# Performance work log

Measured on AMD Instinct MI355X. Metric: run time of the kernel, lower is better.

Reference implementation:

```python
import jax, jax.numpy as jnp
import numpy as np

N_NODES = 100000
N_EDGES = 1600000
IN_FEATS = 128
H_FEATS = 64
PROP_STEP = 2


def _gcn_propagate(x, src, dst, num_nodes, add_self_loops):
    """PyG gcn_norm + scatter-add propagation. edge_weight=None -> all ones.
    GCNConv uses add_self_loops=True; LGConv uses add_self_loops=False."""
    if add_self_loops:
        loop = jnp.arange(num_nodes, dtype=src.dtype)
        src = jnp.concatenate([src, loop])
        dst = jnp.concatenate([dst, loop])
    # degree over destination nodes (flow source_to_target)
    deg = jax.ops.segment_sum(jnp.ones(src.shape, dtype=x.dtype), dst,
                              num_segments=num_nodes)
    dinv = jnp.where(deg > 0, jax.lax.rsqrt(deg), jnp.zeros_like(deg))
    norm = dinv[src] * dinv[dst]                      # [E]
    msg = x[src] * norm[:, None]                      # [E, F] gather + scale
    return jax.ops.segment_sum(msg, dst, num_segments=num_nodes)  # [N, F]


def setup_inputs() -> dict:
    key = jax.random.key(0)
    k1, k2, k3 = jax.random.split(key, 3)
    edge_index = jax.random.randint(k1, (2, N_EDGES), 0, N_NODES, dtype=jnp.int32)
    in_feat = jax.random.normal(k2, (N_NODES, IN_FEATS), dtype=jnp.float32)
    # GCNConv linear weight (bias=False), stored as [in, out]
    W1 = jax.random.normal(k3, (IN_FEATS, H_FEATS), dtype=jnp.float32) * (1.0 / np.sqrt(IN_FEATS))
    alphas = jnp.ones((PROP_STEP,), dtype=jnp.float32)  # nn.Parameter(ones(prop_step))
    return {"edge_index": edge_index, "in_feat": in_feat, "W1": W1, "alphas": alphas}


def reference(edge_index, in_feat, W1, alphas):
    src, dst = edge_index[0], edge_index[1]
    num_nodes = in_feat.shape[0]
    alpha = jax.nn.softmax(alphas)
    # conv1 = GCNConv(bias=False): linear transform then normalized propagation with self loops
    h = _gcn_propagate(in_feat @ W1, src, dst, num_nodes, add_self_loops=True)
    res = h * alpha[0]
    # remaining steps: LGConv (no self loops), norm/relu disabled by default
    for i in range(1, PROP_STEP):
        h = _gcn_propagate(h, src, dst, num_nodes, add_self_loops=False)
        res = res + h * alpha[i]
    return res
```

## Files before the change

kernel.cpp:

```cpp
#include <hip/hip_runtime.h>

#define N_NODES 100000
#define N_EDGES 1600000
#define IN_F 128
#define H_F 64
#define ZROW N_NODES

#define BSH 10
#define BNODES 1024
#define NBKT 98
#define EPB 4096
#define BCAP 20000
#define SCAP 28192

typedef short short8 __attribute__((ext_vector_type(8)));
typedef float floatx4 __attribute__((ext_vector_type(4)));

union U16x8 { short8 v; unsigned short us[8]; unsigned int u[4]; };

static __device__ __forceinline__ unsigned short f2bf(float f) {
    unsigned int u = __float_as_uint(f);
    unsigned int r = (u + 0x7FFFu + ((u >> 16) & 1u)) >> 16;
    return (unsigned short)r;
}
static __device__ __forceinline__ float bflo(unsigned int u) {
    return __uint_as_float(u << 16);
}
static __device__ __forceinline__ float bfhi(unsigned int u) {
    return __uint_as_float(u & 0xFFFF0000u);
}
static __device__ __forceinline__ unsigned int pk2(float a, float b) {
    return (unsigned int)f2bf(a) | ((unsigned int)f2bf(b) << 16);
}

__global__ __launch_bounds__(256) void initwpack_kernel(const float* __restrict__ W,
                                                        unsigned int* __restrict__ wfrag,
                                                        int* __restrict__ ccur,
                                                        unsigned int* __restrict__ XsZ,
                                                        unsigned int* __restrict__ h1sZ) {
    int i = blockIdx.x * 256 + threadIdx.x;
    int reg = i & 3, lane = (i >> 2) & 63, fkc = i >> 8;
    int ct = fkc >> 2, kc = fkc & 3;
    int fcol = ct * 16 + (lane & 15);
    int k = kc * 32 + (lane >> 4) * 8 + reg * 2;
    wfrag[i] = pk2(W[k * 64 + fcol], W[(k + 1) * 64 + fcol]);

    if (blockIdx.x == 0) {
        int t = threadIdx.x;
        if (t < NBKT) ccur[t] = t * BCAP;
        if (t < 32) XsZ[t] = 0;
        else if (t < 64) h1sZ[t - 32] = 0;
    }
}

__global__ __launch_bounds__(256) void coarse_scatter_kernel(const int* __restrict__ src,
                                                             const int* __restrict__ dst,
                                                             int* __restrict__ ccur,
                                                             unsigned int* __restrict__ tmp, int E) {
    __shared__ unsigned int buf[EPB];
    __shared__ unsigned char bktA[EPB];
    __shared__ int cnt[NBKT], lofs[NBKT], gofs[NBKT];
    int base = blockIdx.x * EPB;
    int n = E - base; if (n > EPB) n = EPB;

    for (int i = threadIdx.x; i < NBKT; i += 256) cnt[i] = 0;
    __syncthreads();

    unsigned int v[16]; int bk[16], loc[16];
    #pragma unroll
    for (int j = 0; j < 16; ++j) {
        int o = threadIdx.x + j * 256;
        bk[j] = -1;
        if (o < n) {
            int s = src[base + o];
            int d = dst[base + o];
            bk[j]  = d >> BSH;
            v[j]   = ((unsigned int)(d & (BNODES - 1)) << 17) | (unsigned int)s;
            loc[j] = atomicAdd(&cnt[bk[j]], 1);
        }
    }
    __syncthreads();
    if (threadIdx.x == 0) {
        int run = 0;
        for (int b = 0; b < NBKT; ++b) { lofs[b] = run; run += cnt[b]; }
    }
    __syncthreads();
    if (threadIdx.x < NBKT && cnt[threadIdx.x] > 0)
        gofs[threadIdx.x] = atomicAdd(&ccur[threadIdx.x], cnt[threadIdx.x]);
    __syncthreads();
    #pragma unroll
    for (int j = 0; j < 16; ++j)
        if (bk[j] >= 0) {
            int p = lofs[bk[j]] + loc[j];
            buf[p]  = v[j];
            bktA[p] = (unsigned char)bk[j];
        }
    __syncthreads();
    for (int i = threadIdx.x; i < n; i += 256) {
        int b = bktA[i];
        tmp[gofs[b] + (i - lofs[b])] = buf[i];
    }
}

__global__ __launch_bounds__(512) void bucket_kernel(const unsigned int* __restrict__ tmp,
                                                     const int* __restrict__ ccur,
                                                     unsigned int* __restrict__ meta,
                                                     int* __restrict__ sorted_src,
                                                     float* __restrict__ dinv1,
                                                     float* __restrict__ dinv2, int N) {
    __shared__ int cnt[BNODES];
    __shared__ int sd[512];
    int b   = blockIdx.x;
    int tid = threadIdx.x;
    int tbeg = b * BCAP, tend = ccur[b];
    int sbase = b * SCAP;

    for (int i = tid; i < BNODES; i += 512) cnt[i] = 0;
    __syncthreads();
    for (int i = tbeg + tid; i < tend; i += 512)
        atomicAdd(&cnt[tmp[i] >> 17], 1);
    __syncthreads();

    int c0 = cnt[2 * tid], c1 = cnt[2 * tid + 1];
    int p0 = (c0 + 7) & ~7, p1 = (c1 + 7) & ~7;
    int s  = p0 + p1;
    sd[tid] = s;
    __syncthreads();
    for (int off = 1; off < 512; off <<= 1) {
        int t = (tid >= off) ? sd[tid - off] : 0;
        __syncthreads();
        sd[tid] += t;
        __syncthreads();
    }
    int ex = sd[tid] - s;
    int g0 = sbase + ex, g1 = sbase + ex + p0;

    int node0 = b * BNODES + 2 * tid;
    if (node0 < N) {
        meta[node0] = (unsigned int)g0 | ((unsigned int)(p0 >> 3) << 22);
        dinv1[node0] = rsqrtf((float)(c0 + 1));
        dinv2[node0] = c0 ? rsqrtf((float)c0) : 0.0f;
        for (int k = c0; k < p0; ++k) sorted_src[g0 + k] = ZROW;
    }
    if (node0 + 1 < N) {
        meta[node0 + 1] = (unsigned int)g1 | ((unsigned int)(p1 >> 3) << 22);
        dinv1[node0 + 1] = rsqrtf((float)(c1 + 1));
        dinv2[node0 + 1] = c1 ? rsqrtf((float)c1) : 0.0f;
        for (int k = c1; k < p1; ++k) sorted_src[g1 + k] = ZROW;
    }
    __syncthreads();
    cnt[2 * tid] = g0;
    cnt[2 * tid + 1] = g1;
    __syncthreads();

    for (int i = tbeg + tid; i < tend; i += 512) {
        unsigned int v = tmp[i];
        int p = atomicAdd(&cnt[v >> 17], 1);
        sorted_src[p] = (int)(v & 0x1FFFFu);
    }
}

__global__ __launch_bounds__(256) void gemm_kernel(const float* __restrict__ A,
                                                   const uint4* __restrict__ wfrag,
                                                   const float* __restrict__ dinv1,
                                                   unsigned short* __restrict__ Xs, int nTiles) {
    int wid = blockIdx.x * 4 + (threadIdx.x >> 6);
    int lane = threadIdx.x & 63;
    int lrow = lane & 15, lk = lane >> 4;

    short8 wf[16];
    #pragma unroll
    for (int i = 0; i < 16; ++i)
        wf[i] = *reinterpret_cast<const short8*>(&wfrag[i * 64 + lane]);

    #pragma unroll
    for (int tt = 0; tt < 4; ++tt) {
        int t = wid * 4 + tt;
        if (t >= nTiles) break;
        int node = t * 16 + lrow;
        const float4* ap = reinterpret_cast<const float4*>(A + (size_t)node * IN_F);

        short8 af[4];
        #pragma unroll
        for (int kc = 0; kc < 4; ++kc) {
            float4 x = ap[kc * 8 + lk * 2];
            float4 y = ap[kc * 8 + lk * 2 + 1];
            U16x8 u;
            u.us[0] = f2bf(x.x); u.us[1] = f2bf(x.y); u.us[2] = f2bf(x.z); u.us[3] = f2bf(x.w);
            u.us[4] = f2bf(y.x); u.us[5] = f2bf(y.y); u.us[6] = f2bf(y.z); u.us[7] = f2bf(y.w);
            af[kc] = u.v;
        }

        float dv = dinv1[node];
        #pragma unroll
        for (int ct = 0; ct < 4; ++ct) {
            floatx4 acc = {0.f, 0.f, 0.f, 0.f};
            acc = __builtin_amdgcn_mfma_f32_16x16x32_bf16(wf[ct * 4 + 0], af[0], acc, 0, 0, 0);
            acc = __builtin_amdgcn_mfma_f32_16x16x32_bf16(wf[ct * 4 + 1], af[1], acc, 0, 0, 0);
            acc = __builtin_amdgcn_mfma_f32_16x16x32_bf16(wf[ct * 4 + 2], af[2], acc, 0, 0, 0);
            acc = __builtin_amdgcn_mfma_f32_16x16x32_bf16(wf[ct * 4 + 3], af[3], acc, 0, 0, 0);
            uint2 o;
            o.x = pk2(acc[0] * dv, acc[1] * dv);
            o.y = pk2(acc[2] * dv, acc[3] * dv);
            *reinterpret_cast<uint2*>(Xs + (size_t)node * H_F + ct * 16 + lk * 4) = o;
        }
    }
}

__global__ __launch_bounds__(256) void prop1_kernel(const unsigned int* __restrict__ meta,
                                                    const int* __restrict__ sorted_src,
                                                    const unsigned short* __restrict__ Xs,
                                                    const float* __restrict__ dinv1,
                                                    const float* __restrict__ dinv2,
                                                    unsigned short* __restrict__ h1,
                                                    unsigned short* __restrict__ h1s, int N) {
    int wid  = (blockIdx.x * blockDim.x + threadIdx.x) >> 6;
    int lane = threadIdx.x & 63;
    int g = lane >> 4, fl = lane & 15;
    int d = wid * 4 + g;
    bool active = d < N;
    int dd = active ? d : N - 1;

    unsigned int m = meta[dd];
    int beg = (int)(m & 0x3FFFFFu);
    int nit = (int)(m >> 22);
    const int* idp = sorted_src + beg;
    const char* XsB = (const char*)Xs;
    unsigned bo = (unsigned)(fl << 3);
    float c0 = 0.f, c1 = 0.f, c2 = 0.f, c3 = 0.f;

    for (int it = 0; it < nit; ++it, idp += 8) {
        int s[8]; uint2 v[8];
        #pragma unroll
        for (int j = 0; j < 8; ++j) s[j] = idp[j];
        #pragma unroll
        for (int j = 0; j < 8; ++j)
            v[j] = *reinterpret_cast<const uint2*>(XsB + (((unsigned)s[j] << 7) + bo));
        #pragma unroll
        for (int j = 0; j < 8; ++j) {
            c0 += bflo(v[j].x); c1 += bfhi(v[j].x); c2 += bflo(v[j].y); c3 += bfhi(v[j].y);
        }
    }

    float dv  = dinv1[dd];
    float dv2 = dinv2[dd];
    uint2 sv = *reinterpret_cast<const uint2*>(XsB + (((unsigned)dd << 7) + bo));
    float h0  = dv * (c0 + bflo(sv.x));
    float h1v = dv * (c1 + bfhi(sv.x));
    float h2  = dv * (c2 + bflo(sv.y));
    float h3  = dv * (c3 + bfhi(sv.y));
    if (active) {
        uint2 o1; o1.x = pk2(h0, h1v); o1.y = pk2(h2, h3);
        *reinterpret_cast<uint2*>(h1 + ((size_t)d << 6) + (fl << 2)) = o1;
        uint2 o2; o2.x = pk2(h0 * dv2, h1v * dv2); o2.y = pk2(h2 * dv2, h3 * dv2);
        *reinterpret_cast<uint2*>(h1s + ((size_t)d << 6) + (fl << 2)) = o2;
    }
}

__global__ __launch_bounds__(256) void prop2_kernel(const unsigned int* __restrict__ meta,
                                                    const int* __restrict__ sorted_src,
                                                    const unsigned short* __restrict__ h1,
                                                    const unsigned short* __restrict__ h1s,
                                                    const float* __restrict__ dinv2,
                                                    const float* __restrict__ alphas,
                                                    float* __restrict__ out, int N) {
    int wid  = (blockIdx.x * blockDim.x + threadIdx.x) >> 6;
    int lane = threadIdx.x & 63;
    int g = lane >> 4, fl = lane & 15;
    int d = wid * 4 + g;
    bool active = d < N;
    int dd = active ? d : N - 1;

    float e0 = expf(alphas[0]), e1 = expf(alphas[1]);
    float aw0 = e0 / (e0 + e1), aw1 = e1 / (e0 + e1);

    unsigned int m = meta[dd];
    int beg = (int)(m & 0x3FFFFFu);
    int nit = (int)(m >> 22);
    const int* idp = sorted_src + beg;
    const char* HB = (const char*)h1s;
    unsigned bo = (unsigned)(fl << 3);
    float c0 = 0.f, c1 = 0.f, c2 = 0.f, c3 = 0.f;

    for (int it = 0; it < nit; ++it, idp += 8) {
        int s[8]; uint2 v[8];
        #pragma unroll
        for (int j = 0; j < 8; ++j) s[j] = idp[j];
        #pragma unroll
        for (int j = 0; j < 8; ++j)
            v[j] = *reinterpret_cast<const uint2*>(HB + (((unsigned)s[j] << 7) + bo));
        #pragma unroll
        for (int j = 0; j < 8; ++j) {
            c0 += bflo(v[j].x); c1 += bfhi(v[j].x); c2 += bflo(v[j].y); c3 += bfhi(v[j].y);
        }
    }

    if (active) {
        float sa1 = aw1 * dinv2[dd];
        uint2 sv = *reinterpret_cast<const uint2*>((const char*)h1 + (((unsigned)d << 7) + bo));
        float4 o;
        o.x = aw0 * bflo(sv.x) + sa1 * c0;
        o.y = aw0 * bfhi(sv.x) + sa1 * c1;
        o.z = aw0 * bflo(sv.y) + sa1 * c2;
        o.w = aw0 * bfhi(sv.y) + sa1 * c3;
        *reinterpret_cast<float4*>(out + ((size_t)d << 6) + (fl << 2)) = o;
    }
}

extern "C" void kernel_launch(void* const* d_in, const int* in_sizes, int n_in,
                              void* d_out, int out_size, void* d_ws, size_t ws_size,
                              hipStream_t stream) {
    const int*   edge_index = (const int*)d_in[0];
    const float* in_feat    = (const float*)d_in[1];
    const float* W1         = (const float*)d_in[2];
    const float* alphas     = (const float*)d_in[3];
    float*       out        = (float*)d_out;

    const int* src = edge_index;
    const int* dst = edge_index + N_EDGES;

    char* ws = (char*)d_ws;
    size_t tabBytes = (size_t)(N_NODES + 16) * H_F * 2;
    unsigned short* Xs  = (unsigned short*)(ws);
    unsigned int*   tmp = (unsigned int*)(ws);
    unsigned short* h1  = (unsigned short*)(ws + tabBytes);
    unsigned short* h1s = (unsigned short*)(ws + 2 * tabBytes);
    char* p = ws + 3 * tabBytes;
    int*   sorted = (int*)p;   p += (size_t)NBKT * SCAP * 4;
    unsigned int* meta = (unsigned int*)p; p += (size_t)(N_NODES + 4) * 4;
    float* dinv1  = (float*)p; p += (size_t)N_NODES * 4;
    float* dinv2  = (float*)p; p += (size_t)N_NODES * 4;
    int*   ccur   = (int*)p;   p += (size_t)NBKT * 4;
    unsigned int* wfrag = (unsigned int*)p; p += 8192 * 4;

    initwpack_kernel<<<32, 256, 0, stream>>>(W1, wfrag, ccur,
                                             (unsigned int*)(Xs + (size_t)N_NODES * H_F),
                                             (unsigned int*)(h1s + (size_t)N_NODES * H_F));
    coarse_scatter_kernel<<<(N_EDGES + EPB - 1) / EPB, 256, 0, stream>>>(src, dst, ccur, tmp, N_EDGES);
    bucket_kernel<<<NBKT, 512, 0, stream>>>(tmp, ccur, meta, sorted, dinv1, dinv2, N_NODES);

    int nTiles = N_NODES / 16;
    int gemm_waves = (nTiles + 3) / 4;
    gemm_kernel<<<(gemm_waves + 3) / 4, 256, 0, stream>>>(in_feat, (const uint4*)wfrag, dinv1, Xs, nTiles);

    int pwaves  = (N_NODES + 3) / 4;
    int pblocks = (pwaves + 3) / 4;
    prop1_kernel<<<pblocks, 256, 0, stream>>>(meta, sorted, Xs, dinv1, dinv2, h1, h1s, N_NODES);
    prop2_kernel<<<pblocks, 256, 0, stream>>>(meta, sorted, h1, h1s, dinv2, alphas, out, N_NODES);
}
```

Measured before the change: 131.6 us.

## Split feature tables into four 16-column slices for cache-local gathers

Stores Xs, h1 and h1s as four separate 16-feature slices (32 bytes per node per slice). Propagation kernels launch one grid per slice, so each gathered table is a quarter of its former size and more likely to stay resident in L2/MALL. Within a wave, groups of four lanes now split a destination's edge list and reduce partial sums with cross-lane shuffles. In exchange, the edge index lists are re-read four times, more blocks are launched, and each gather moves only 32-byte rows.

```diff
diff --git a/kernel.cpp b/kernel.cpp
--- a/kernel.cpp
+++ b/kernel.cpp
@@ -13,6 +13,9 @@
 #define BCAP 20000
 #define SCAP 28192
 
+#define NSLICE 4
+#define SLICE_ELEMS ((size_t)(N_NODES + 16) * 16)
+
 typedef short short8 __attribute__((ext_vector_type(8)));
 typedef float floatx4 __attribute__((ext_vector_type(4)));
 
@@ -36,8 +39,7 @@
 __global__ __launch_bounds__(256) void initwpack_kernel(const float* __restrict__ W,
                                                         unsigned int* __restrict__ wfrag,
                                                         int* __restrict__ ccur,
-                                                        unsigned int* __restrict__ XsZ,
-                                                        unsigned int* __restrict__ h1sZ) {
+                                                        unsigned short* __restrict__ h1sS) {
     int i = blockIdx.x * 256 + threadIdx.x;
     int reg = i & 3, lane = (i >> 2) & 63, fkc = i >> 8;
     int ct = fkc >> 2, kc = fkc & 3;
@@ -48,8 +50,11 @@
     if (blockIdx.x == 0) {
         int t = threadIdx.x;
         if (t < NBKT) ccur[t] = t * BCAP;
-        if (t < 32) XsZ[t] = 0;
-        else if (t < 64) h1sZ[t - 32] = 0;
+        if (t < 32) {
+            unsigned int* w = (unsigned int*)(h1sS + (size_t)(t >> 3) * SLICE_ELEMS
+                                              + (size_t)ZROW * 16);
+            w[t & 7] = 0;
+        }
     }
 }
 
@@ -163,7 +168,14 @@
 __global__ __launch_bounds__(256) void gemm_kernel(const float* __restrict__ A,
                                                    const uint4* __restrict__ wfrag,
                                                    const float* __restrict__ dinv1,
-                                                   unsigned short* __restrict__ Xs, int nTiles) {
+                                                   unsigned short* __restrict__ XsS, int nTiles) {
+    if (blockIdx.x == 0 && threadIdx.x < 32) {
+        int t = threadIdx.x;
+        unsigned int* w = (unsigned int*)(XsS + (size_t)(t >> 3) * SLICE_ELEMS
+                                          + (size_t)ZROW * 16);
+        w[t & 7] = 0;
+    }
+
     int wid = blockIdx.x * 4 + (threadIdx.x >> 6);
     int lane = threadIdx.x & 63;
     int lrow = lane & 15, lk = lane >> 4;
@@ -202,21 +214,26 @@
             uint2 o;
             o.x = pk2(acc[0] * dv, acc[1] * dv);
             o.y = pk2(acc[2] * dv, acc[3] * dv);
-            *reinterpret_cast<uint2*>(Xs + (size_t)node * H_F + ct * 16 + lk * 4) = o;
+            *reinterpret_cast<uint2*>(XsS + (size_t)ct * SLICE_ELEMS + (size_t)node * 16 + lk * 4) = o;
         }
     }
 }
 
 __global__ __launch_bounds__(256) void prop1_kernel(const unsigned int* __restrict__ meta,
                                                     const int* __restrict__ sorted_src,
-                                                    const unsigned short* __restrict__ Xs,
+                                                    const unsigned short* __restrict__ XsS,
                                                     const float* __restrict__ dinv1,
                                                     const float* __restrict__ dinv2,
-                                                    unsigned short* __restrict__ h1,
-                                                    unsigned short* __restrict__ h1s, int N) {
-    int wid  = (blockIdx.x * blockDim.x + threadIdx.x) >> 6;
-    int lane = threadIdx.x & 63;
-    int g = lane >> 4, fl = lane & 15;
+                                                    unsigned short* __restrict__ h1S,
+                                                    unsigned short* __restrict__ h1sS,
+                                                    int N, int pblocks) {
+    int slice = blockIdx.x / pblocks;
+    int bx    = blockIdx.x - slice * pblocks;
+    int wid   = bx * 4 + (threadIdx.x >> 6);
+    int lane  = threadIdx.x & 63;
+    int g  = lane >> 4, j = lane & 15;
+    int es = j >> 2;
+    unsigned bo = (unsigned)((j & 3) << 3);
     int d = wid * 4 + g;
     bool active = d < N;
     int dd = active ? d : N - 1;
@@ -225,48 +242,66 @@
     int beg = (int)(m & 0x3FFFFFu);
     int nit = (int)(m >> 22);
     const int* idp = sorted_src + beg;
-    const char* XsB = (const char*)Xs;
-    unsigned bo = (unsigned)(fl << 3);
+    const char* XB = (const char*)(XsS + (size_t)slice * SLICE_ELEMS);
     float c0 = 0.f, c1 = 0.f, c2 = 0.f, c3 = 0.f;
 
-    for (int it = 0; it < nit; ++it, idp += 8) {
-        int s[8]; uint2 v[8];
-        #pragma unroll
-        for (int j = 0; j < 8; ++j) s[j] = idp[j];
-        #pragma unroll
-        for (int j = 0; j < 8; ++j)
-            v[j] = *reinterpret_cast<const uint2*>(XsB + (((unsigned)s[j] << 7) + bo));
-        #pragma unroll
-        for (int j = 0; j < 8; ++j) {
-            c0 += bflo(v[j].x); c1 += bfhi(v[j].x); c2 += bflo(v[j].y); c3 += bfhi(v[j].y);
-        }
-    }
+    int it = 0;
+    for (; it + 2 <= nit; it += 2, idp += 16) {
+        int s0 = idp[es], s1 = idp[4 + es], s2 = idp[8 + es], s3 = idp[12 + es];
+        uint2 v0 = *reinterpret_cast<const uint2*>(XB + (((unsigned)s0 << 5) + bo));
+        uint2 v1 = *reinterpret_cast<const uint2*>(XB + (((unsigned)s1 << 5) + bo));
+        uint2 v2 = *reinterpret_cast<const uint2*>(XB + (((unsigned)s2 << 5) + bo));
+        uint2 v3 = *reinterpret_cast<const uint2*>(XB + (((unsigned)s3 << 5) + bo));
+        c0 += bflo(v0.x); c1 += bfhi(v0.x); c2 += bflo(v0.y); c3 += bfhi(v0.y);
+        c0 += bflo(v1.x); c1 += bfhi(v1.x); c2 += bflo(v1.y); c3 += bfhi(v1.y);
+        c0 += bflo(v2.x); c1 += bfhi(v2.x); c2 += bflo(v2.y); c3 += bfhi(v2.y);
+        c0 += bflo(v3.x); c1 += bfhi(v3.x); c2 += bflo(v3.y); c3 += bfhi(v3.y);
+    }
+    if (it < nit) {
+        int s0 = idp[es], s1 = idp[4 + es];
+        uint2 v0 = *reinterpret_cast<const uint2*>(XB + (((unsigned)s0 << 5) + bo));
+        uint2 v1 = *reinterpret_cast<const uint2*>(XB + (((unsigned)s1 << 5) + bo));
+        c0 += bflo(v0.x); c1 += bfhi(v0.x); c2 += bflo(v0.y); c3 += bfhi(v0.y);
+        c0 += bflo(v1.x); c1 += bfhi(v1.x); c2 += bflo(v1.y); c3 += bfhi(v1.y);
+    }
+
+    c0 += __shfl_xor(c0, 4); c1 += __shfl_xor(c1, 4);
+    c2 += __shfl_xor(c2, 4); c3 += __shfl_xor(c3, 4);
+    c0 += __shfl_xor(c0, 8); c1 += __shfl_xor(c1, 8);
+    c2 += __shfl_xor(c2, 8); c3 += __shfl_xor(c3, 8);
 
     float dv  = dinv1[dd];
     float dv2 = dinv2[dd];
-    uint2 sv = *reinterpret_cast<const uint2*>(XsB + (((unsigned)dd << 7) + bo));
+    uint2 sv = *reinterpret_cast<const uint2*>(XB + (((unsigned)dd << 5) + bo));
     float h0  = dv * (c0 + bflo(sv.x));
     float h1v = dv * (c1 + bfhi(sv.x));
     float h2  = dv * (c2 + bflo(sv.y));
     float h3  = dv * (c3 + bfhi(sv.y));
-    if (active) {
+    if (active && es == 0) {
+        char* HB  = (char*)h1S  + (size_t)slice * SLICE_ELEMS * 2;
+        char* HSB = (char*)h1sS + (size_t)slice * SLICE_ELEMS * 2;
         uint2 o1; o1.x = pk2(h0, h1v); o1.y = pk2(h2, h3);
-        *reinterpret_cast<uint2*>(h1 + ((size_t)d << 6) + (fl << 2)) = o1;
+        *reinterpret_cast<uint2*>(HB + (((unsigned)d << 5) + bo)) = o1;
         uint2 o2; o2.x = pk2(h0 * dv2, h1v * dv2); o2.y = pk2(h2 * dv2, h3 * dv2);
-        *reinterpret_cast<uint2*>(h1s + ((size_t)d << 6) + (fl << 2)) = o2;
+        *reinterpret_cast<uint2*>(HSB + (((unsigned)d << 5) + bo)) = o2;
     }
 }
 
 __global__ __launch_bounds__(256) void prop2_kernel(const unsigned int* __restrict__ meta,
                                                     const int* __restrict__ sorted_src,
-                                                    const unsigned short* __restrict__ h1,
-                                                    const unsigned short* __restrict__ h1s,
+                                                    const unsigned short* __restrict__ h1S,
+                                                    const unsigned short* __restrict__ h1sS,
                                                     const float* __restrict__ dinv2,
                                                     const float* __restrict__ alphas,
-                                                    float* __restrict__ out, int N) {
-    int wid  = (blockIdx.x * blockDim.x + threadIdx.x) >> 6;
-    int lane = threadIdx.x & 63;
-    int g = lane >> 4, fl = lane & 15;
+                                                    float* __restrict__ out,
+                                                    int N, int pblocks) {
+    int slice = blockIdx.x / pblocks;
+    int bx    = blockIdx.x - slice * pblocks;
+    int wid   = bx * 4 + (threadIdx.x >> 6);
+    int lane  = threadIdx.x & 63;
+    int g  = lane >> 4, j = lane & 15;
+    int es = j >> 2;
+    unsigned bo = (unsigned)((j & 3) << 3);
     int d = wid * 4 + g;
     bool active = d < N;
     int dd = active ? d : N - 1;
@@ -278,32 +313,44 @@
     int beg = (int)(m & 0x3FFFFFu);
     int nit = (int)(m >> 22);
     const int* idp = sorted_src + beg;
-    const char* HB = (const char*)h1s;
-    unsigned bo = (unsigned)(fl << 3);
+    const char* HSB = (const char*)(h1sS + (size_t)slice * SLICE_ELEMS);
     float c0 = 0.f, c1 = 0.f, c2 = 0.f, c3 = 0.f;
 
-    for (int it = 0; it < nit; ++it, idp += 8) {
-        int s[8]; uint2 v[8];
-        #pragma unroll
-        for (int j = 0; j < 8; ++j) s[j] = idp[j];
-        #pragma unroll
-        for (int j = 0; j < 8; ++j)
-            v[j] = *reinterpret_cast<const uint2*>(HB + (((unsigned)s[j] << 7) + bo));
-        #pragma unroll
-        for (int j = 0; j < 8; ++j) {
-            c0 += bflo(v[j].x); c1 += bfhi(v[j].x); c2 += bflo(v[j].y); c3 += bfhi(v[j].y);
-        }
-    }
-
-    if (active) {
+    int it = 0;
+    for (; it + 2 <= nit; it += 2, idp += 16) {
+        int s0 = idp[es], s1 = idp[4 + es], s2 = idp[8 + es], s3 = idp[12 + es];
+        uint2 v0 = *reinterpret_cast<const uint2*>(HSB + (((unsigned)s0 << 5) + bo));
+        uint2 v1 = *reinterpret_cast<const uint2*>(HSB + (((unsigned)s1 << 5) + bo));
+        uint2 v2 = *reinterpret_cast<const uint2*>(HSB + (((unsigned)s2 << 5) + bo));
+        uint2 v3 = *reinterpret_cast<const uint2*>(HSB + (((unsigned)s3 << 5) + bo));
+        c0 += bflo(v0.x); c1 += bfhi(v0.x); c2 += bflo(v0.y); c3 += bfhi(v0.y);
+        c0 += bflo(v1.x); c1 += bfhi(v1.x); c2 += bflo(v1.y); c3 += bfhi(v1.y);
+        c0 += bflo(v2.x); c1 += bfhi(v2.x); c2 += bflo(v2.y); c3 += bfhi(v2.y);
+        c0 += bflo(v3.x); c1 += bfhi(v3.x); c2 += bflo(v3.y); c3 += bfhi(v3.y);
+    }
+    if (it < nit) {
+        int s0 = idp[es], s1 = idp[4 + es];
+        uint2 v0 = *reinterpret_cast<const uint2*>(HSB + (((unsigned)s0 << 5) + bo));
+        uint2 v1 = *reinterpret_cast<const uint2*>(HSB + (((unsigned)s1 << 5) + bo));
+        c0 += bflo(v0.x); c1 += bfhi(v0.x); c2 += bflo(v0.y); c3 += bfhi(v0.y);
+        c0 += bflo(v1.x); c1 += bfhi(v1.x); c2 += bflo(v1.y); c3 += bfhi(v1.y);
+    }
+
+    c0 += __shfl_xor(c0, 4); c1 += __shfl_xor(c1, 4);
+    c2 += __shfl_xor(c2, 4); c3 += __shfl_xor(c3, 4);
+    c0 += __shfl_xor(c0, 8); c1 += __shfl_xor(c1, 8);
+    c2 += __shfl_xor(c2, 8); c3 += __shfl_xor(c3, 8);
+
+    if (active && es == 0) {
         float sa1 = aw1 * dinv2[dd];
-        uint2 sv = *reinterpret_cast<const uint2*>((const char*)h1 + (((unsigned)d << 7) + bo));
+        const char* HB = (const char*)(h1S + (size_t)slice * SLICE_ELEMS);
+        uint2 sv = *reinterpret_cast<const uint2*>(HB + (((unsigned)d << 5) + bo));
         float4 o;
         o.x = aw0 * bflo(sv.x) + sa1 * c0;
         o.y = aw0 * bfhi(sv.x) + sa1 * c1;
         o.z = aw0 * bflo(sv.y) + sa1 * c2;
         o.w = aw0 * bfhi(sv.y) + sa1 * c3;
-        *reinterpret_cast<float4*>(out + ((size_t)d << 6) + (fl << 2)) = o;
+        *reinterpret_cast<float4*>(out + (size_t)d * H_F + slice * 16 + (j & 3) * 4) = o;
     }
 }
 
@@ -320,11 +367,11 @@
     const int* dst = edge_index + N_EDGES;
 
     char* ws = (char*)d_ws;
-    size_t tabBytes = (size_t)(N_NODES + 16) * H_F * 2;
-    unsigned short* Xs  = (unsigned short*)(ws);
-    unsigned int*   tmp = (unsigned int*)(ws);
-    unsigned short* h1  = (unsigned short*)(ws + tabBytes);
-    unsigned short* h1s = (unsigned short*)(ws + 2 * tabBytes);
+    size_t tabBytes = (size_t)NSLICE * SLICE_ELEMS * 2;
+    unsigned short* XsS  = (unsigned short*)(ws);
+    unsigned int*   tmp  = (unsigned int*)(ws);
+    unsigned short* h1S  = (unsigned short*)(ws + tabBytes);
+    unsigned short* h1sS = (unsigned short*)(ws + 2 * tabBytes);
     char* p = ws + 3 * tabBytes;
     int*   sorted = (int*)p;   p += (size_t)NBKT * SCAP * 4;
     unsigned int* meta = (unsigned int*)p; p += (size_t)(N_NODES + 4) * 4;
@@ -333,18 +380,18 @@
     int*   ccur   = (int*)p;   p += (size_t)NBKT * 4;
     unsigned int* wfrag = (unsigned int*)p; p += 8192 * 4;
 
-    initwpack_kernel<<<32, 256, 0, stream>>>(W1, wfrag, ccur,
-                                             (unsigned int*)(Xs + (size_t)N_NODES * H_F),
-                                             (unsigned int*)(h1s + (size_t)N_NODES * H_F));
+    initwpack_kernel<<<32, 256, 0, stream>>>(W1, wfrag, ccur, h1sS);
     coarse_scatter_kernel<<<(N_EDGES + EPB - 1) / EPB, 256, 0, stream>>>(src, dst, ccur, tmp, N_EDGES);
     bucket_kernel<<<NBKT, 512, 0, stream>>>(tmp, ccur, meta, sorted, dinv1, dinv2, N_NODES);
 
     int nTiles = N_NODES / 16;
     int gemm_waves = (nTiles + 3) / 4;
-    gemm_kernel<<<(gemm_waves + 3) / 4, 256, 0, stream>>>(in_feat, (const uint4*)wfrag, dinv1, Xs, nTiles);
+    gemm_kernel<<<(gemm_waves + 3) / 4, 256, 0, stream>>>(in_feat, (const uint4*)wfrag, dinv1, XsS, nTiles);
 
     int pwaves  = (N_NODES + 3) / 4;
     int pblocks = (pwaves + 3) / 4;
-    prop1_kernel<<<pblocks, 256, 0, stream>>>(meta, sorted, Xs, dinv1, dinv2, h1, h1s, N_NODES);
-    prop2_kernel<<<pblocks, 256, 0, stream>>>(meta, sorted, h1, h1s, dinv2, alphas, out, N_NODES);
-}
+    prop1_kernel<<<NSLICE * pblocks, 256, 0, stream>>>(meta, sorted, XsS, dinv1, dinv2,
+                                                       h1S, h1sS, N_NODES, pblocks);
+    prop2_kernel<<<NSLICE * pblocks, 256, 0, stream>>>(meta, sorted, h1S, h1sS, dinv2,
+                                                       alphas, out, N_NODES, pblocks);
+}
```

Measured after the change: 168.9 us. 28.4% more time.
